# Performance work log

Measured on AMD Instinct MI355X. Metric: run time of the kernel, lower is better.

## Reference

```python
import jax, jax.numpy as jnp
import numpy as np

EMB_DIM = 64
NUM_USERS = 1_000_000
NUM_ITEMS = 1_000_000
NUM_GROUPS = 100_000
NUM_MEMBERS = 3_200_000
BATCH = 16_384


def setup_inputs() -> dict:
    key = jax.random.key(0)
    ks = jax.random.split(key, 10)
    # xavier-uniform-ish embedding tables
    bound_u = float(np.sqrt(6.0 / (NUM_USERS + EMB_DIM)))
    bound_i = float(np.sqrt(6.0 / (NUM_ITEMS + EMB_DIM)))
    user_emb = jax.random.uniform(ks[0], (NUM_USERS, EMB_DIM), jnp.float32, -bound_u, bound_u)
    item_emb = jax.random.uniform(ks[1], (NUM_ITEMS, EMB_DIM), jnp.float32, -bound_i, bound_i)
    # PredictLayer: Linear(emb_dim, 8) -> ReLU -> Linear(8, 1)
    w1 = jax.random.normal(ks[2], (EMB_DIM, 8), jnp.float32) * (1.0 / np.sqrt(EMB_DIM))
    b1 = jnp.zeros((8,), jnp.float32)
    w2 = jax.random.normal(ks[3], (8, 1), jnp.float32) * (1.0 / np.sqrt(8))
    b2 = jnp.zeros((1,), jnp.float32)
    # flattened ragged group_number_dict: member i of group member_groups[i] is user member_users[i]
    member_users = jax.random.randint(ks[4], (NUM_MEMBERS,), 0, NUM_USERS)
    member_groups = jnp.sort(jax.random.randint(ks[5], (NUM_MEMBERS,), 0, NUM_GROUPS))
    group_inputs = jax.random.randint(ks[6], (BATCH,), 0, NUM_GROUPS)
    item_inputs = jax.random.randint(ks[7], (BATCH,), 0, NUM_ITEMS)
    return {
        "user_emb": user_emb, "item_emb": item_emb,
        "w1": w1, "b1": b1, "w2": w2, "b2": b2,
        "member_users": member_users, "member_groups": member_groups,
        "group_inputs": group_inputs, "item_inputs": item_inputs,
        "num_groups": NUM_GROUPS,
    }


def reference(user_emb, item_emb, w1, b1, w2, b2,
              member_users, member_groups, group_inputs, item_inputs, num_groups):
    # segment-mean of user embeddings per group (replaces the per-group python loop)
    member_emb = user_emb[member_users]                       # [M, D] gather
    sums = jax.ops.segment_sum(member_emb, member_groups,
                               num_segments=num_groups, indices_are_sorted=True)   # [G, D]
    counts = jax.ops.segment_sum(jnp.ones(member_users.shape, user_emb.dtype), member_groups,
                                 num_segments=num_groups, indices_are_sorted=True)  # [G]
    group_mean = sums / jnp.maximum(counts, 1.0)[:, None]     # [G, D]
    g_emb = group_mean[group_inputs]                          # [B, D]
    i_emb = item_emb[item_inputs]                             # [B, D]
    x = g_emb * i_emb                                         # [B, D]
    h = jax.nn.relu(x @ w1 + b1)                              # [B, 8]
    return jax.nn.sigmoid(h @ w2 + b2)                        # [B, 1]
```

## Files before the change

### kernel.cpp

```cpp
#include <hip/hip_runtime.h>
#include <math.h>

#define EMB 64

__global__ __launch_bounds__(256) void consrec_kernel(
    const float* __restrict__ user_emb,
    const float* __restrict__ item_emb,
    const float* __restrict__ w1,
    const float* __restrict__ b1,
    const float* __restrict__ w2,
    const float* __restrict__ b2,
    const int*   __restrict__ member_users,
    const int*   __restrict__ member_groups,
    const int*   __restrict__ group_inputs,
    const int*   __restrict__ item_inputs,
    int num_members,
    int batch,
    float* __restrict__ out)
{
    const int wave = (int)((blockIdx.x * blockDim.x + threadIdx.x) >> 6);
    const int lane = threadIdx.x & 63;
    if (wave >= batch) return;

    const int g = group_inputs[wave];

    int lo = 0, hi = num_members;
    while (lo < hi) {
        int mid = (lo + hi) >> 1;
        if (member_groups[mid] < g) lo = mid + 1; else hi = mid;
    }
    const int start = lo;
    hi = num_members;
    while (lo < hi) {
        int mid = (lo + hi) >> 1;
        if (member_groups[mid] <= g) lo = mid + 1; else hi = mid;
    }
    const int end = lo;

    float sum = 0.f;
    for (int j = start; j < end; ++j) {
        const int u = member_users[j];
        sum += user_emb[(size_t)u * EMB + lane];
    }
    const int cnt = end - start;
    const float mean = sum / (float)(cnt > 0 ? cnt : 1);

    const float x = mean * item_emb[(size_t)item_inputs[wave] * EMB + lane];

    float p[8];
    #pragma unroll
    for (int k = 0; k < 8; ++k) p[k] = x * w1[lane * 8 + k];

    #pragma unroll
    for (int off = 32; off >= 1; off >>= 1) {
        #pragma unroll
        for (int k = 0; k < 8; ++k) p[k] += __shfl_xor(p[k], off, 64);
    }

    float acc = b2[0];
    #pragma unroll
    for (int k = 0; k < 8; ++k) {
        float h = p[k] + b1[k];
        h = h > 0.f ? h : 0.f;
        acc += h * w2[k];
    }
    const float y = 1.f / (1.f + expf(-acc));
    if (lane == 0) out[wave] = y;
}

extern "C" void kernel_launch(void* const* d_in, const int* in_sizes, int n_in,
                              void* d_out, int out_size, void* d_ws, size_t ws_size,
                              hipStream_t stream) {
    const float* user_emb      = (const float*)d_in[0];
    const float* item_emb      = (const float*)d_in[1];
    const float* w1            = (const float*)d_in[2];
    const float* b1            = (const float*)d_in[3];
    const float* w2            = (const float*)d_in[4];
    const float* b2            = (const float*)d_in[5];
    const int*   member_users  = (const int*)d_in[6];
    const int*   member_groups = (const int*)d_in[7];
    const int*   group_inputs  = (const int*)d_in[8];
    const int*   item_inputs   = (const int*)d_in[9];

    const int num_members = in_sizes[6];
    const int batch       = in_sizes[8];

    const int threads = 256;
    const int waves_per_block = threads / 64;
    const int grid = (batch + waves_per_block - 1) / waves_per_block;

    consrec_kernel<<<grid, threads, 0, stream>>>(
        user_emb, item_emb, w1, b1, w2, b2,
        member_users, member_groups, group_inputs, item_inputs,
        num_members, batch, (float*)d_out);
}
```

Measured before the change: 521.1 us.

## Precompute group offsets with a boundary kernel and batch member gathers via readlane

Adds a pre-pass kernel that turns the sorted member_groups array into a CSR offsets array in workspace. Each wave then reads its start and end in two loads instead of doing two binary searches over 3.2M entries. The member loop now loads up to 64 member ids coalesced per wave, broadcasts them with readlane, and unrolls by four so several embedding-row loads are in flight together. The cost is an extra launch and a full pass over member_groups each call, plus reliance on the num_groups input living on the device.

```diff
diff --git a/kernel.cpp b/kernel.cpp
--- a/kernel.cpp
+++ b/kernel.cpp
@@ -2,6 +2,27 @@
 #include <math.h>
 
 #define EMB 64
+
+__global__ __launch_bounds__(256) void boundaries_kernel(
+    const int* __restrict__ member_groups,
+    int num_members,
+    const int* __restrict__ num_groups_p,
+    int* __restrict__ offs)
+{
+    const int j = blockIdx.x * blockDim.x + threadIdx.x;
+    if (j >= num_members) return;
+    const int gj = member_groups[j];
+    if (j == 0) {
+        for (int g = 0; g <= gj; ++g) offs[g] = 0;
+    } else {
+        const int gp = member_groups[j - 1];
+        for (int g = gp + 1; g <= gj; ++g) offs[g] = j;
+    }
+    if (j == num_members - 1) {
+        const int G = *num_groups_p;
+        for (int g = gj + 1; g <= G; ++g) offs[g] = num_members;
+    }
+}
 
 __global__ __launch_bounds__(256) void consrec_kernel(
     const float* __restrict__ user_emb,
@@ -11,10 +32,9 @@
     const float* __restrict__ w2,
     const float* __restrict__ b2,
     const int*   __restrict__ member_users,
-    const int*   __restrict__ member_groups,
+    const int*   __restrict__ offs,
     const int*   __restrict__ group_inputs,
     const int*   __restrict__ item_inputs,
-    int num_members,
     int batch,
     float* __restrict__ out)
 {
@@ -22,27 +42,32 @@
     const int lane = threadIdx.x & 63;
     if (wave >= batch) return;
 
-    const int g = group_inputs[wave];
-
-    int lo = 0, hi = num_members;
-    while (lo < hi) {
-        int mid = (lo + hi) >> 1;
-        if (member_groups[mid] < g) lo = mid + 1; else hi = mid;
-    }
-    const int start = lo;
-    hi = num_members;
-    while (lo < hi) {
-        int mid = (lo + hi) >> 1;
-        if (member_groups[mid] <= g) lo = mid + 1; else hi = mid;
-    }
-    const int end = lo;
+    const int g     = group_inputs[wave];
+    const int start = offs[g];
+    const int end   = offs[g + 1];
+    const int cnt   = end - start;
 
     float sum = 0.f;
-    for (int j = start; j < end; ++j) {
-        const int u = member_users[j];
-        sum += user_emb[(size_t)u * EMB + lane];
+    for (int base = start; base < end; base += 64) {
+        const int m = min(64, end - base);
+        const int uvec = (lane < m) ? member_users[base + lane] : 0;
+        int j = 0;
+        for (; j + 4 <= m; j += 4) {
+            const int u0 = __builtin_amdgcn_readlane(uvec, j + 0);
+            const int u1 = __builtin_amdgcn_readlane(uvec, j + 1);
+            const int u2 = __builtin_amdgcn_readlane(uvec, j + 2);
+            const int u3 = __builtin_amdgcn_readlane(uvec, j + 3);
+            const float a0 = user_emb[((size_t)u0 << 6) + lane];
+            const float a1 = user_emb[((size_t)u1 << 6) + lane];
+            const float a2 = user_emb[((size_t)u2 << 6) + lane];
+            const float a3 = user_emb[((size_t)u3 << 6) + lane];
+            sum += a0; sum += a1; sum += a2; sum += a3;
+        }
+        for (; j < m; ++j) {
+            const int u = __builtin_amdgcn_readlane(uvec, j);
+            sum += user_emb[((size_t)u << 6) + lane];
+        }
     }
-    const int cnt = end - start;
     const float mean = sum / (float)(cnt > 0 ? cnt : 1);
 
     const float x = mean * item_emb[(size_t)item_inputs[wave] * EMB + lane];
@@ -81,16 +106,26 @@
     const int*   member_groups = (const int*)d_in[7];
     const int*   group_inputs  = (const int*)d_in[8];
     const int*   item_inputs   = (const int*)d_in[9];
+    const int*   num_groups_p  = (const int*)d_in[10];
 
     const int num_members = in_sizes[6];
     const int batch       = in_sizes[8];
 
-    const int threads = 256;
-    const int waves_per_block = threads / 64;
-    const int grid = (batch + waves_per_block - 1) / waves_per_block;
+    int* offs = (int*)d_ws;
 
-    consrec_kernel<<<grid, threads, 0, stream>>>(
-        user_emb, item_emb, w1, b1, w2, b2,
-        member_users, member_groups, group_inputs, item_inputs,
-        num_members, batch, (float*)d_out);
+    {
+        const int threads = 256;
+        const int grid = (num_members + threads - 1) / threads;
+        boundaries_kernel<<<grid, threads, 0, stream>>>(
+            member_groups, num_members, num_groups_p, offs);
+    }
+    {
+        const int threads = 256;
+        const int waves_per_block = threads / 64;
+        const int grid = (batch + waves_per_block - 1) / waves_per_block;
+        consrec_kernel<<<grid, threads, 0, stream>>>(
+            user_emb, item_emb, w1, b1, w2, b2,
+            member_users, offs, group_inputs, item_inputs,
+            batch, (float*)d_out);
+    }
 }
```

New measurement: 443.4 us. -14.9%, faster.
